# Performance work log

Hardware: AMD Instinct MI355X
Metric: run time of the kernel (lower is better)

Reference implementation:

```python
import jax, jax.numpy as jnp
import numpy as np

E, B, D, H, Z = 8, 16384, 512, 512, 64   # experts, batch, input_dim, hidden, latent
NHID = 2                                 # num_mlp_layers - 1 hidden-to-hidden layers


def setup_inputs() -> dict:
    key = jax.random.key(0)
    ks = jax.random.split(key, 12)

    def w(k, shape, fan_in):
        return (jax.random.normal(k, shape, jnp.float32) / np.sqrt(fan_in)).astype(jnp.float32)

    return {
        "x": jax.random.normal(ks[0], (B, D), jnp.float32),
        "eps": jax.random.normal(ks[1], (B, Z), jnp.float32),
        # stacked per-expert parameters (leading axis E)
        "enc_in_w": w(ks[2], (E, D, H), D), "enc_in_b": jnp.zeros((E, H), jnp.float32),
        "enc_hid_w": w(ks[3], (E, NHID, H, H), H), "enc_hid_b": jnp.zeros((E, NHID, H), jnp.float32),
        "mu_w": w(ks[4], (E, H, Z), H), "mu_b": jnp.zeros((E, Z), jnp.float32),
        "lv_w": w(ks[5], (E, H, Z), H), "lv_b": jnp.zeros((E, Z), jnp.float32),
        "dec_in_w": w(ks[6], (E, Z, H), Z), "dec_in_b": jnp.zeros((E, H), jnp.float32),
        "dec_hid_w": w(ks[7], (E, NHID, H, H), H), "dec_hid_b": jnp.zeros((E, NHID, H), jnp.float32),
        "dec_out_w": w(ks[8], (E, H, D), H), "dec_out_b": jnp.zeros((E, D), jnp.float32),
    }


def _moe_forward(x, eps, enc_in_w, enc_in_b, enc_hid_w, enc_hid_b,
                 mu_w, mu_b, lv_w, lv_b,
                 dec_in_w, dec_in_b, dec_hid_w, dec_hid_b, dec_out_w, dec_out_b):
    # ---- every expert tries the problem (dense, all experts over full batch) ----
    h = jax.nn.relu(jnp.einsum('bd,edh->ebh', x, enc_in_w) + enc_in_b[:, None, :])
    for i in range(NHID):
        h = jax.nn.relu(jnp.einsum('ebh,ehk->ebk', h, enc_hid_w[:, i]) + enc_hid_b[:, i, None, :])
    mu = jnp.einsum('ebh,ehz->ebz', h, mu_w) + mu_b[:, None, :]          # [E,B,Z]
    logvar = jnp.einsum('ebh,ehz->ebz', h, lv_w) + lv_b[:, None, :]       # [E,B,Z]
    z = mu + jnp.exp(0.5 * logvar) * eps[None, :, :]                      # reparameterize
    g = jax.nn.relu(jnp.einsum('ebz,ezh->ebh', z, dec_in_w) + dec_in_b[:, None, :])
    for i in range(NHID):
        g = jax.nn.relu(jnp.einsum('ebh,ehk->ebk', g, dec_hid_w[:, i]) + dec_hid_b[:, i, None, :])
    xhat = jnp.einsum('ebh,ehd->ebd', g, dec_out_w) + dec_out_b[:, None, :]  # [E,B,D]

    # ---- per-sample recon loss, pick best expert (torch.min over experts) ----
    recon = jnp.mean((xhat - x[None, :, :]) ** 2, axis=-1)                # [E,B]
    expert_idx = jnp.argmin(recon, axis=0)                                # [B]

    # ---- sparse_others: single fused gather instead of python loop ----
    bi = jnp.arange(x.shape[0])
    return mu[expert_idx, bi], logvar[expert_idx, bi], xhat[expert_idx, bi]


def reference(x, eps, enc_in_w, enc_in_b, enc_hid_w, enc_hid_b,
              mu_w, mu_b, lv_w, lv_b,
              dec_in_w, dec_in_b, dec_hid_w, dec_hid_b, dec_out_w, dec_out_b):
    return _moe_forward(x, eps, enc_in_w, enc_in_b, enc_hid_w, enc_hid_b,
                        mu_w, mu_b, lv_w, lv_b,
                        dec_in_w, dec_in_b, dec_hid_w, dec_hid_b, dec_out_w, dec_out_b)
```

## Files before the change

### kernel.cpp

```cpp
#include <hip/hip_runtime.h>
#include <cstdint>

#define Eexp 8
#define Bb   16384
#define Dd   512
#define Hh   512
#define Zz   64

typedef _Float16 f16x8 __attribute__((ext_vector_type(8)));
typedef float    f32x4 __attribute__((ext_vector_type(4)));

#define OFF_ENCIN  0
#define OFF_HID0   524288
#define OFF_HID1   1048576
#define OFF_HEADS  1572864
#define OFF_DECIN  1703936
#define OFF_DHID0  1769472
#define OFF_DHID1  2293760
#define OFF_DECOUT 2818048
#define PEREXP     3342336
#define WT_TOTAL   (8 * (size_t)PEREXP)

template<bool TR>
__global__ __launch_bounds__(256)
void fmsplit(const float* __restrict__ src, _Float16* __restrict__ dst,
             int KTOT, int inner, long sStride, long dStride)
{
    __shared__ float t[64][65];
    const int e  = blockIdx.z;
    const int o0 = blockIdx.x * 64;
    const int k0 = blockIdx.y * 64;
    const float* S = src + (size_t)e * sStride;
    _Float16*    D = dst + (size_t)e * dStride;
    const int tid = threadIdx.x;
    const int rr = tid >> 4, c4 = (tid & 15) * 4;
    #pragma unroll
    for (int p = 0; p < 4; ++p) {
        const int r = rr + p * 16;
        const float4 v = *reinterpret_cast<const float4*>(
            S + (size_t)(TR ? (k0 + r) : (o0 + r)) * inner + (TR ? o0 : k0) + c4);
        t[r][c4 + 0] = v.x; t[r][c4 + 1] = v.y;
        t[r][c4 + 2] = v.z; t[r][c4 + 3] = v.w;
    }
    __syncthreads();
    const int lane = tid & 63, wid = tid >> 6;
    #pragma unroll
    for (int p = 0; p < 2; ++p) {
        const int g  = wid * 2 + p;
        const int ot = g >> 1, kb = g & 1;
        const int ridx  = ot * 16 + (lane & 15);
        const int kbase = kb * 32 + (lane >> 4) * 8;
        f16x8 hv, lvv;
        #pragma unroll
        for (int j = 0; j < 8; ++j) {
            const float v = TR ? t[kbase + j][ridx] : t[ridx][kbase + j];
            const _Float16 h = (_Float16)v;
            hv[j]  = h;
            lvv[j] = (_Float16)(v - (float)h);
        }
        const size_t base =
            ((size_t)((o0 >> 4) + ot) * (KTOT >> 5) + (k0 >> 5) + kb) * 1024;
        *reinterpret_cast<f16x8*>(D + base + lane * 8)       = hv;
        *reinterpret_cast<f16x8*>(D + base + 512 + lane * 8) = lvv;
    }
}

__global__ __launch_bounds__(256)
void zfm_kernel(const float* __restrict__ mu, const float* __restrict__ lv,
                const float* __restrict__ eps, _Float16* __restrict__ zfm)
{
    __shared__ float t[64][65];
    const int r0 = blockIdx.x * 64;
    const int tid = threadIdx.x, rr = tid >> 4, c4 = (tid & 15) * 4;
    #pragma unroll
    for (int p = 0; p < 4; ++p) {
        const int r = rr + p * 16;
        const size_t o = (size_t)(r0 + r) * 64 + c4;
        const float4 m = *reinterpret_cast<const float4*>(mu + o);
        const float4 l = *reinterpret_cast<const float4*>(lv + o);
        const float4 e = *reinterpret_cast<const float4*>(eps + o);
        t[r][c4 + 0] = m.x + expf(0.5f * l.x) * e.x;
        t[r][c4 + 1] = m.y + expf(0.5f * l.y) * e.y;
        t[r][c4 + 2] = m.z + expf(0.5f * l.z) * e.z;
        t[r][c4 + 3] = m.w + expf(0.5f * l.w) * e.w;
    }
    __syncthreads();
    const int lane = tid & 63, wid = tid >> 6;
    #pragma unroll
    for (int p = 0; p < 2; ++p) {
        const int g  = wid * 2 + p;
        const int ot = g >> 1, kb = g & 1;
        const int ridx  = ot * 16 + (lane & 15);
        const int kbase = kb * 32 + (lane >> 4) * 8;
        f16x8 hv, lvv;
        #pragma unroll
        for (int j = 0; j < 8; ++j) {
            const float v = t[ridx][kbase + j];
            const _Float16 h = (_Float16)v;
            hv[j]  = h;
            lvv[j] = (_Float16)(v - (float)h);
        }
        const size_t base = ((size_t)((r0 >> 4) + ot) * 2 + kb) * 1024;
        *reinterpret_cast<f16x8*>(zfm + base + lane * 8)       = hv;
        *reinterpret_cast<f16x8*>(zfm + base + 512 + lane * 8) = lvv;
    }
}

template<int KA, int MODE>
__global__ __launch_bounds__(256, 3)
void gemm6(const _Float16* __restrict__ Afm, const _Float16* __restrict__ Wfm,
           const float* __restrict__ bias0, const float* __restrict__ bias1,
           float* __restrict__ Cf, float* __restrict__ Cf1,
           _Float16* __restrict__ Cfm,
           const float* __restrict__ Xin, float* __restrict__ rec8)
{
    constexpr int nY = (MODE == 2) ? 1 : 4;
    constexpr int KB = KA / 32;
    __shared__ uint32_t sb[(MODE == 0) ? 2 * 4096 : 64];

    int wg = blockIdx.x;
    wg = (wg & 7) * ((int)gridDim.x >> 3) + (wg >> 3);
    const int bx = wg / nY, by = wg % nY;

    const int lane = threadIdx.x & 63, wid = threadIdx.x >> 6;
    const int wr = wid >> 1, wc = wid & 1;
    const int row0 = bx * 128, col0 = by * 128;
    const int rt0 = (row0 >> 4) + wr * 4;
    const int ct0 = (col0 >> 4) + wc * 4;

    const _Float16* aBase = Afm + (size_t)rt0 * KB * 1024 + lane * 8;
    const _Float16* wBase = Wfm + (size_t)ct0 * KB * 1024 + lane * 8;

    f32x4 acc[4][4];
    #pragma unroll
    for (int i = 0; i < 4; ++i)
        #pragma unroll
        for (int j = 0; j < 4; ++j) acc[i][j] = {0.f, 0.f, 0.f, 0.f};

    for (int kb = 0; kb < KB; ++kb) {
        f16x8 ah[4], al[4], wh[4], wl[4];
        #pragma unroll
        for (int mf = 0; mf < 4; ++mf) {
            const _Float16* p = aBase + ((size_t)mf * KB + kb) * 1024;
            ah[mf] = *reinterpret_cast<const f16x8*>(p);
            al[mf] = *reinterpret_cast<const f16x8*>(p + 512);
        }
        #pragma unroll
        for (int nf = 0; nf < 4; ++nf) {
            const _Float16* p = wBase + ((size_t)nf * KB + kb) * 1024;
            wh[nf] = *reinterpret_cast<const f16x8*>(p);
            wl[nf] = *reinterpret_cast<const f16x8*>(p + 512);
        }
        #pragma unroll
        for (int mf = 0; mf < 4; ++mf)
            #pragma unroll
            for (int nf = 0; nf < 4; ++nf) {
                acc[mf][nf] = __builtin_amdgcn_mfma_f32_16x16x32_f16(
                    ah[mf], wh[nf], acc[mf][nf], 0, 0, 0);
                acc[mf][nf] = __builtin_amdgcn_mfma_f32_16x16x32_f16(
                    ah[mf], wl[nf], acc[mf][nf], 0, 0, 0);
                acc[mf][nf] = __builtin_amdgcn_mfma_f32_16x16x32_f16(
                    al[mf], wh[nf], acc[mf][nf], 0, 0, 0);
            }
    }

    if (MODE == 0) {
        #pragma unroll
        for (int p = 0; p < 2; ++p) {
            if (wc == p) {
                #pragma unroll
                for (int nf = 0; nf < 4; ++nf) {
                    const int col = nf * 16 + (lane & 15);
                    const float bv = bias0[col0 + wc * 64 + col];
                    #pragma unroll
                    for (int mf = 0; mf < 4; ++mf)
                        #pragma unroll
                        for (int j = 0; j < 4; ++j) {
                            const int lrow = mf * 16 + (lane >> 4) * 4 + j;
                            const float v = fmaxf(acc[mf][nf][j] + bv, 0.f);
                            const _Float16 h = (_Float16)v;
                            const _Float16 l = (_Float16)(v - (float)h);
                            const uint32_t pk =
                                (uint32_t)__builtin_bit_cast(uint16_t, h) |
                                ((uint32_t)__builtin_bit_cast(uint16_t, l) << 16);
                            const int chunk = (col >> 2) ^ (lrow & 15);
                            sb[wr * 4096 + lrow * 64 + chunk * 4 + (col & 3)] = pk;
                        }
                }
            }
            __syncthreads();
            if (wc == p) {
                #pragma unroll
                for (int t4 = 0; t4 < 4; ++t4)
                    #pragma unroll
                    for (int kb2 = 0; kb2 < 2; ++kb2) {
                        const int lrow = t4 * 16 + (lane & 15);
                        uint32_t u[8];
                        #pragma unroll
                        for (int jb = 0; jb < 2; ++jb) {
                            const int chunk =
                                (kb2 * 8 + (lane >> 4) * 2 + jb) ^ (lrow & 15);
                            const uint32_t* pp =
                                &sb[wr * 4096 + lrow * 64 + chunk * 4];
                            u[jb * 4 + 0] = pp[0]; u[jb * 4 + 1] = pp[1];
                            u[jb * 4 + 2] = pp[2]; u[jb * 4 + 3] = pp[3];
                        }
                        f16x8 hv, lvv;
                        #pragma unroll
                        for (int j = 0; j < 8; ++j) {
                            hv[j]  = __builtin_bit_cast(_Float16, (uint16_t)(u[j] & 0xffff));
                            lvv[j] = __builtin_bit_cast(_Float16, (uint16_t)(u[j] >> 16));
                        }
                        const int gtile = (row0 >> 4) + wr * 4 + t4;
                        const int gkb   = (col0 >> 5) + wc * 2 + kb2;
                        const size_t base = ((size_t)gtile * 16 + gkb) * 1024;
                        *reinterpret_cast<f16x8*>(Cfm + base + lane * 8)       = hv;
                        *reinterpret_cast<f16x8*>(Cfm + base + 512 + lane * 8) = lvv;
                    }
            }
            __syncthreads();
        }
    } else if (MODE == 1) {
        float rsum[4][4];
        #pragma unroll
        for (int mf = 0; mf < 4; ++mf)
            #pragma unroll
            for (int j = 0; j < 4; ++j) rsum[mf][j] = 0.f;
        #pragma unroll
        for (int nf = 0; nf < 4; ++nf) {
            const int col = col0 + wc * 64 + nf * 16 + (lane & 15);
            const float bv = bias0[col];
            #pragma unroll
            for (int mf = 0; mf < 4; ++mf)
                #pragma unroll
                for (int j = 0; j < 4; ++j) {
                    const int row = row0 + wr * 64 + mf * 16 + (lane >> 4) * 4 + j;
                    const float v = acc[mf][nf][j] + bv;
                    Cf[(size_t)row * 512 + col] = v;
                    const float d = v - Xin[(size_t)row * 512 + col];
                    rsum[mf][j] += d * d;
                }
        }
        #pragma unroll
        for (int mf = 0; mf < 4; ++mf)
            #pragma unroll
            for (int j = 0; j < 4; ++j) {
                float s = rsum[mf][j];
                s += __shfl_xor(s, 1); s += __shfl_xor(s, 2);
                s += __shfl_xor(s, 4); s += __shfl_xor(s, 8);
                if ((lane & 15) == 0) {
                    const int row = row0 + wr * 64 + mf * 16 + (lane >> 4) * 4 + j;
                    rec8[(size_t)(by * 2 + wc) * Bb + row] = s;
                }
            }
    } else {
        #pragma unroll
        for (int nf = 0; nf < 4; ++nf) {
            const int colq = wc * 64 + nf * 16 + (lane & 15);
            const float bv = (colq < 64) ? bias0[colq] : bias1[colq - 64];
            float* CP = (colq < 64) ? Cf : Cf1;
            const int c = colq & 63;
            #pragma unroll
            for (int mf = 0; mf < 4; ++mf)
                #pragma unroll
                for (int j = 0; j < 4; ++j) {
                    const int row = row0 + wr * 64 + mf * 16 + (lane >> 4) * 4 + j;
                    CP[(size_t)row * 64 + c] = acc[mf][nf][j] + bv;
                }
        }
    }
}

__global__ __launch_bounds__(256)
void select_kernel(const float* __restrict__ rec8, float* __restrict__ best,
                   const float* __restrict__ mu_e, const float* __restrict__ lv_e,
                   const float* __restrict__ xhat,
                   float* __restrict__ out_mu, float* __restrict__ out_lv,
                   float* __restrict__ out_xh, int isFirst)
{
    const int wave = threadIdx.x >> 6;
    const int lane = threadIdx.x & 63;
    const int row  = blockIdx.x * 4 + wave;
    float r = 0.f;
    #pragma unroll
    for (int p = 0; p < 8; ++p) r += rec8[(size_t)p * Bb + row];
    r *= (1.0f / 512.0f);
    const bool cond = isFirst || (r < best[row]);
    if (cond) {
        if (lane == 0) best[row] = r;
        out_mu[(size_t)row * Zz + lane] = mu_e[(size_t)row * Zz + lane];
        out_lv[(size_t)row * Zz + lane] = lv_e[(size_t)row * Zz + lane];
        const float4* src = reinterpret_cast<const float4*>(&xhat[(size_t)row * Dd]);
        float4*       dst = reinterpret_cast<float4*>(&out_xh[(size_t)row * Dd]);
        dst[lane]      = src[lane];
        dst[lane + 64] = src[lane + 64];
    }
}

extern "C" void kernel_launch(void* const* d_in, const int* in_sizes, int n_in,
                              void* d_out, int out_size, void* d_ws, size_t ws_size,
                              hipStream_t stream)
{
    const float* x         = (const float*)d_in[0];
    const float* eps       = (const float*)d_in[1];
    const float* enc_in_w  = (const float*)d_in[2];
    const float* enc_in_b  = (const float*)d_in[3];
    const float* enc_hid_w = (const float*)d_in[4];
    const float* enc_hid_b = (const float*)d_in[5];
    const float* mu_w      = (const float*)d_in[6];
    const float* mu_b      = (const float*)d_in[7];
    const float* lv_w      = (const float*)d_in[8];
    const float* lv_b      = (const float*)d_in[9];
    const float* dec_in_w  = (const float*)d_in[10];
    const float* dec_in_b  = (const float*)d_in[11];
    const float* dec_hid_w = (const float*)d_in[12];
    const float* dec_hid_b = (const float*)d_in[13];
    const float* dec_out_w = (const float*)d_in[14];
    const float* dec_out_b = (const float*)d_in[15];

    const size_t FM = (size_t)Bb * 512 * 2;
    const size_t BZ = (size_t)Bb * 64;

    _Float16* wt  = (_Float16*)d_ws;
    _Float16* xfm = wt + WT_TOTAL;
    _Float16* afm = xfm + FM;
    _Float16* bfm = afm + FM;
    _Float16* zfm = bfm + FM;
    float* fbase  = (float*)(zfm + (size_t)Bb * 64 * 2);
    float* xhat   = fbase;
    float* mu_e   = xhat + (size_t)Bb * 512;
    float* lv_e   = mu_e + BZ;
    float* rec8   = lv_e + BZ;
    float* best   = rec8 + (size_t)8 * Bb;

    float* out_mu = (float*)d_out;
    float* out_lv = out_mu + (size_t)Bb * Zz;
    float* out_xh = out_lv + (size_t)Bb * Zz;

    const dim3 blk(256);

    fmsplit<true ><<<dim3(8, 8, 8), blk, 0, stream>>>(enc_in_w,           wt + OFF_ENCIN,  512, 512, 262144, PEREXP);
    fmsplit<true ><<<dim3(8, 8, 8), blk, 0, stream>>>(enc_hid_w,          wt + OFF_HID0,   512, 512, 524288, PEREXP);
    fmsplit<true ><<<dim3(8, 8, 8), blk, 0, stream>>>(enc_hid_w + 262144, wt + OFF_HID1,   512, 512, 524288, PEREXP);
    fmsplit<true ><<<dim3(1, 8, 8), blk, 0, stream>>>(mu_w,               wt + OFF_HEADS,  512,  64,  32768, PEREXP);
    fmsplit<true ><<<dim3(1, 8, 8), blk, 0, stream>>>(lv_w,   wt + OFF_HEADS + 65536,      512,  64,  32768, PEREXP);
    fmsplit<true ><<<dim3(8, 1, 8), blk, 0, stream>>>(dec_in_w,           wt + OFF_DECIN,   64, 512,  32768, PEREXP);
    fmsplit<true ><<<dim3(8, 8, 8), blk, 0, stream>>>(dec_hid_w,          wt + OFF_DHID0,  512, 512, 524288, PEREXP);
    fmsplit<true ><<<dim3(8, 8, 8), blk, 0, stream>>>(dec_hid_w + 262144, wt + OFF_DHID1,  512, 512, 524288, PEREXP);
    fmsplit<true ><<<dim3(8, 8, 8), blk, 0, stream>>>(dec_out_w,          wt + OFF_DECOUT, 512, 512, 262144, PEREXP);
    fmsplit<false><<<dim3(256, 8, 1), blk, 0, stream>>>(x,                xfm,             512, 512, 0, 0);

    const dim3 gBig(512), gHead(128), gRow(Bb / 4), gZ(Bb / 64);

    for (int e = 0; e < Eexp; ++e) {
        const _Float16* we = wt + (size_t)e * PEREXP;
        gemm6<512, 0><<<gBig, blk, 0, stream>>>(
            xfm, we + OFF_ENCIN, enc_in_b + (size_t)e * Hh, nullptr,
            nullptr, nullptr, afm, nullptr, nullptr);
        gemm6<512, 0><<<gBig, blk, 0, stream>>>(
            afm, we + OFF_HID0, enc_hid_b + ((size_t)e * 2 + 0) * Hh, nullptr,
            nullptr, nullptr, bfm, nullptr, nullptr);
        gemm6<512, 0><<<gBig, blk, 0, stream>>>(
            bfm, we + OFF_HID1, enc_hid_b + ((size_t)e * 2 + 1) * Hh, nullptr,
            nullptr, nullptr, afm, nullptr, nullptr);
        gemm6<512, 2><<<gHead, blk, 0, stream>>>(
            afm, we + OFF_HEADS, mu_b + (size_t)e * Zz, lv_b + (size_t)e * Zz,
            mu_e, lv_e, nullptr, nullptr, nullptr);
        zfm_kernel<<<gZ, blk, 0, stream>>>(mu_e, lv_e, eps, zfm);
        gemm6< 64, 0><<<gBig, blk, 0, stream>>>(
            zfm, we + OFF_DECIN, dec_in_b + (size_t)e * Hh, nullptr,
            nullptr, nullptr, bfm, nullptr, nullptr);
        gemm6<512, 0><<<gBig, blk, 0, stream>>>(
            bfm, we + OFF_DHID0, dec_hid_b + ((size_t)e * 2 + 0) * Hh, nullptr,
            nullptr, nullptr, afm, nullptr, nullptr);
        gemm6<512, 0><<<gBig, blk, 0, stream>>>(
            afm, we + OFF_DHID1, dec_hid_b + ((size_t)e * 2 + 1) * Hh, nullptr,
            nullptr, nullptr, bfm, nullptr, nullptr);
        gemm6<512, 1><<<gBig, blk, 0, stream>>>(
            bfm, we + OFF_DECOUT, dec_out_b + (size_t)e * Dd, nullptr,
            xhat, nullptr, nullptr, x, rec8);
        select_kernel<<<gRow, blk, 0, stream>>>(
            rec8, best, mu_e, lv_e, xhat, out_mu, out_lv, out_xh, e == 0 ? 1 : 0);
    }
}
```

Before: 1.891 ms.

## Rewrite GEMM with 32x32 MFMA, LDS-staged weights and double-buffered pipeline

Replaces the 16x16x32 MFMA GEMM with one built on 32x32x16 MFMA, using 512-thread blocks and a fragment-major layout regrouped into 32-row, 16-k tiles. Weight tiles are staged into LDS through global_load_lds double buffering, and activation fragments are register double-buffered, with explicit waitcnt/barrier ordering and setprio around the MFMA bursts. The aim is to reuse weight tiles across waves and to overlap global loads with compute, so redundant per-wave global weight loads go away. In exchange the code carries tighter hand-written synchronisation, and the block-index swizzle for L2 locality is removed.

Result: slower. 2.057 ms (+8.8%).

```diff
diff --git a/kernel.cpp b/kernel.cpp
--- a/kernel.cpp
+++ b/kernel.cpp
@@ -7,8 +7,8 @@
 #define Hh   512
 #define Zz   64
 
-typedef _Float16 f16x8 __attribute__((ext_vector_type(8)));
-typedef float    f32x4 __attribute__((ext_vector_type(4)));
+typedef _Float16 f16x8  __attribute__((ext_vector_type(8)));
+typedef float    f32x16 __attribute__((ext_vector_type(16)));
 
 #define OFF_ENCIN  0
 #define OFF_HID0   524288
@@ -20,6 +20,10 @@
 #define OFF_DECOUT 2818048
 #define PEREXP     3342336
 #define WT_TOTAL   (8 * (size_t)PEREXP)
+
+#define GLL16(g, l) __builtin_amdgcn_global_load_lds( \
+    (const __attribute__((address_space(1))) void*)(g), \
+    (__attribute__((address_space(3))) void*)(l), 16, 0, 0)
 
 template<bool TR>
 __global__ __launch_bounds__(256)
@@ -44,24 +48,23 @@
     }
     __syncthreads();
     const int lane = tid & 63, wid = tid >> 6;
+    const int KB = KTOT >> 4;
     #pragma unroll
     for (int p = 0; p < 2; ++p) {
         const int g  = wid * 2 + p;
-        const int ot = g >> 1, kb = g & 1;
-        const int ridx  = ot * 16 + (lane & 15);
-        const int kbase = kb * 32 + (lane >> 4) * 8;
-        f16x8 hv, lvv;
+        const int ot = g >> 2, kk = g & 3;
+        const int rI = ot * 32 + (lane & 31);
+        const int kI = kk * 16 + (lane >> 5) * 8;
+        f16x8 hv, lv;
         #pragma unroll
         for (int j = 0; j < 8; ++j) {
-            const float v = TR ? t[kbase + j][ridx] : t[ridx][kbase + j];
+            const float v = TR ? t[kI + j][rI] : t[rI][kI + j];
             const _Float16 h = (_Float16)v;
-            hv[j]  = h;
-            lvv[j] = (_Float16)(v - (float)h);
+            hv[j] = h; lv[j] = (_Float16)(v - (float)h);
         }
-        const size_t base =
-            ((size_t)((o0 >> 4) + ot) * (KTOT >> 5) + (k0 >> 5) + kb) * 1024;
+        const size_t base = ((size_t)((o0 >> 5) + ot) * KB + (k0 >> 4) + kk) * 1024;
         *reinterpret_cast<f16x8*>(D + base + lane * 8)       = hv;
-        *reinterpret_cast<f16x8*>(D + base + 512 + lane * 8) = lvv;
+        *reinterpret_cast<f16x8*>(D + base + 512 + lane * 8) = lv;
     }
 }
 
@@ -89,121 +92,188 @@
     #pragma unroll
     for (int p = 0; p < 2; ++p) {
         const int g  = wid * 2 + p;
-        const int ot = g >> 1, kb = g & 1;
-        const int ridx  = ot * 16 + (lane & 15);
-        const int kbase = kb * 32 + (lane >> 4) * 8;
+        const int ot = g >> 2, kk = g & 3;
+        const int rI = ot * 32 + (lane & 31);
+        const int kI = kk * 16 + (lane >> 5) * 8;
         f16x8 hv, lvv;
         #pragma unroll
         for (int j = 0; j < 8; ++j) {
-            const float v = t[ridx][kbase + j];
+            const float v = t[rI][kI + j];
             const _Float16 h = (_Float16)v;
-            hv[j]  = h;
-            lvv[j] = (_Float16)(v - (float)h);
+            hv[j] = h; lvv[j] = (_Float16)(v - (float)h);
         }
-        const size_t base = ((size_t)((r0 >> 4) + ot) * 2 + kb) * 1024;
+        const size_t base = ((size_t)((r0 >> 5) + ot) * 4 + kk) * 1024;
         *reinterpret_cast<f16x8*>(zfm + base + lane * 8)       = hv;
         *reinterpret_cast<f16x8*>(zfm + base + 512 + lane * 8) = lvv;
     }
 }
 
 template<int KA, int MODE>
-__global__ __launch_bounds__(256, 3)
-void gemm6(const _Float16* __restrict__ Afm, const _Float16* __restrict__ Wfm,
+__global__ __launch_bounds__(512, 2)
+void gemm7(const _Float16* __restrict__ Afm, const _Float16* __restrict__ Wfm,
            const float* __restrict__ bias0, const float* __restrict__ bias1,
            float* __restrict__ Cf, float* __restrict__ Cf1,
            _Float16* __restrict__ Cfm,
            const float* __restrict__ Xin, float* __restrict__ rec8)
 {
-    constexpr int nY = (MODE == 2) ? 1 : 4;
-    constexpr int KB = KA / 32;
-    __shared__ uint32_t sb[(MODE == 0) ? 2 * 4096 : 64];
-
-    int wg = blockIdx.x;
-    wg = (wg & 7) * ((int)gridDim.x >> 3) + (wg >> 3);
+    constexpr int TM   = (MODE == 2) ? 1 : 2;
+    constexpr int TN   = (MODE == 2) ? 1 : 2;
+    constexpr int nY   = (MODE == 2) ? 2 : 4;
+    constexpr int BN32 = (MODE == 2) ? 2 : 4;
+    constexpr int KB   = KA / 16;
+    constexpr int NT   = KA / 32;
+    constexpr int CH   = BN32 * 4;
+    constexpr int CPW  = CH / 8;
+    constexpr int LDSB = (MODE == 0) ? 65536 : 2 * CH * 1024;
+    __shared__ __align__(16) uint8_t lds_raw[LDSB];
+    _Float16* sW = reinterpret_cast<_Float16*>(lds_raw);
+
+    const int wg = blockIdx.x;
     const int bx = wg / nY, by = wg % nY;
-
     const int lane = threadIdx.x & 63, wid = threadIdx.x >> 6;
     const int wr = wid >> 1, wc = wid & 1;
-    const int row0 = bx * 128, col0 = by * 128;
-    const int rt0 = (row0 >> 4) + wr * 4;
-    const int ct0 = (col0 >> 4) + wc * 4;
-
-    const _Float16* aBase = Afm + (size_t)rt0 * KB * 1024 + lane * 8;
-    const _Float16* wBase = Wfm + (size_t)ct0 * KB * 1024 + lane * 8;
-
-    f32x4 acc[4][4];
-    #pragma unroll
-    for (int i = 0; i < 4; ++i)
-        #pragma unroll
-        for (int j = 0; j < 4; ++j) acc[i][j] = {0.f, 0.f, 0.f, 0.f};
-
-    for (int kb = 0; kb < KB; ++kb) {
-        f16x8 ah[4], al[4], wh[4], wl[4];
-        #pragma unroll
-        for (int mf = 0; mf < 4; ++mf) {
-            const _Float16* p = aBase + ((size_t)mf * KB + kb) * 1024;
-            ah[mf] = *reinterpret_cast<const f16x8*>(p);
-            al[mf] = *reinterpret_cast<const f16x8*>(p + 512);
-        }
-        #pragma unroll
-        for (int nf = 0; nf < 4; ++nf) {
-            const _Float16* p = wBase + ((size_t)nf * KB + kb) * 1024;
-            wh[nf] = *reinterpret_cast<const f16x8*>(p);
-            wl[nf] = *reinterpret_cast<const f16x8*>(p + 512);
-        }
-        #pragma unroll
-        for (int mf = 0; mf < 4; ++mf)
+
+    const int rt0  = bx * (TM * 4) + wr * TM;
+    const int ct0  = by * BN32;
+    const int col0 = by * (BN32 * 32);
+
+    const _Float16* wSrc[CPW];
+    #pragma unroll
+    for (int p = 0; p < CPW; ++p) {
+        const int q  = wid * CPW + p;
+        const int wt = q >> 2, s = (q >> 1) & 1, pl = q & 1;
+        wSrc[p] = Wfm + ((size_t)(ct0 + wt) * KB + s) * 1024 + pl * 512 + lane * 8;
+    }
+    const _Float16* aSrc[TM];
+    #pragma unroll
+    for (int mf = 0; mf < TM; ++mf)
+        aSrc[mf] = Afm + (size_t)(rt0 + mf) * KB * 1024 + lane * 8;
+
+    f32x16 acc[TM][TN];
+    #pragma unroll
+    for (int i = 0; i < TM; ++i)
+        #pragma unroll
+        for (int j = 0; j < TN; ++j)
             #pragma unroll
-            for (int nf = 0; nf < 4; ++nf) {
-                acc[mf][nf] = __builtin_amdgcn_mfma_f32_16x16x32_f16(
-                    ah[mf], wh[nf], acc[mf][nf], 0, 0, 0);
-                acc[mf][nf] = __builtin_amdgcn_mfma_f32_16x16x32_f16(
-                    ah[mf], wl[nf], acc[mf][nf], 0, 0, 0);
-                acc[mf][nf] = __builtin_amdgcn_mfma_f32_16x16x32_f16(
-                    al[mf], wh[nf], acc[mf][nf], 0, 0, 0);
-            }
-    }
-
-    if (MODE == 0) {
-        #pragma unroll
-        for (int p = 0; p < 2; ++p) {
-            if (wc == p) {
+            for (int r = 0; r < 16; ++r) acc[i][j][r] = 0.f;
+
+    f16x8 aRegA[TM][2][2], aRegB[TM][2][2];
+
+#define STAGE_W(buf)                                                          \
+    { _Pragma("unroll")                                                       \
+      for (int p = 0; p < CPW; ++p) {                                         \
+          GLL16(wSrc[p], sW + (buf) * (CH * 512) + (wid * CPW + p) * 512);    \
+          wSrc[p] += 2048;                                                    \
+      } }
+
+#define LOAD_A(dst)                                                           \
+    { _Pragma("unroll")                                                       \
+      for (int mf = 0; mf < TM; ++mf) {                                       \
+          _Pragma("unroll")                                                   \
+          for (int s = 0; s < 2; ++s)                                         \
+              _Pragma("unroll")                                               \
+              for (int pl = 0; pl < 2; ++pl)                                  \
+                  dst[mf][s][pl] = *reinterpret_cast<const f16x8*>(           \
+                      aSrc[mf] + s * 1024 + pl * 512);                        \
+          aSrc[mf] += 2048;                                                   \
+      } }
+
+    STAGE_W(0)
+    LOAD_A(aRegA)
+    if (NT > 1) STAGE_W(1)
+
+#define ITER(t, buf, aCur, aNxt)                                              \
+    {                                                                         \
+        if ((t) + 1 < NT) {                                                   \
+            if constexpr (CPW == 2)                                           \
+                asm volatile("s_waitcnt vmcnt(2)" ::: "memory");              \
+            else                                                              \
+                asm volatile("s_waitcnt vmcnt(1)" ::: "memory");              \
+        } else {                                                              \
+            asm volatile("s_waitcnt vmcnt(0)" ::: "memory");                  \
+        }                                                                     \
+        __builtin_amdgcn_s_barrier();                                         \
+        asm volatile("" ::: "memory");                                        \
+        if ((t) + 1 < NT) LOAD_A(aNxt)                                        \
+        f16x8 wf[TN][2][2];                                                   \
+        _Pragma("unroll")                                                     \
+        for (int nf = 0; nf < TN; ++nf)                                       \
+            _Pragma("unroll")                                                 \
+            for (int s = 0; s < 2; ++s)                                       \
+                _Pragma("unroll")                                             \
+                for (int pl = 0; pl < 2; ++pl)                                \
+                    wf[nf][s][pl] = *reinterpret_cast<const f16x8*>(          \
+                        sW + (buf) * (CH * 512) +                             \
+                        (((wc * TN + nf) * 2 + s) * 2 + pl) * 512 + lane * 8);\
+        __builtin_amdgcn_s_setprio(1);                                        \
+        _Pragma("unroll")                                                     \
+        for (int s = 0; s < 2; ++s)                                           \
+            _Pragma("unroll")                                                 \
+            for (int mf = 0; mf < TM; ++mf)                                   \
+                _Pragma("unroll")                                             \
+                for (int nf = 0; nf < TN; ++nf) {                             \
+                    acc[mf][nf] = __builtin_amdgcn_mfma_f32_32x32x16_f16(     \
+                        aCur[mf][s][0], wf[nf][s][0], acc[mf][nf], 0, 0, 0);  \
+                    acc[mf][nf] = __builtin_amdgcn_mfma_f32_32x32x16_f16(     \
+                        aCur[mf][s][0], wf[nf][s][1], acc[mf][nf], 0, 0, 0);  \
+                    acc[mf][nf] = __builtin_amdgcn_mfma_f32_32x32x16_f16(     \
+                        aCur[mf][s][1], wf[nf][s][0], acc[mf][nf], 0, 0, 0);  \
+                }                                                             \
+        __builtin_amdgcn_s_setprio(0);                                        \
+        asm volatile("" ::: "memory");                                        \
+        __builtin_amdgcn_s_barrier();                                         \
+        asm volatile("" ::: "memory");                                        \
+        if ((t) + 2 < NT) STAGE_W(buf)                                        \
+    }
+
+    for (int t = 0; t < NT; t += 2) {
+        ITER(t,     0, aRegA, aRegB)
+        ITER(t + 1, 1, aRegB, aRegA)
+    }
+#undef ITER
+#undef LOAD_A
+#undef STAGE_W
+
+    if constexpr (MODE == 0) {
+        uint32_t* sb = reinterpret_cast<uint32_t*>(lds_raw);
+        #pragma unroll
+        for (int ph = 0; ph < 2; ++ph) {
+            if (wc == ph) {
                 #pragma unroll
-                for (int nf = 0; nf < 4; ++nf) {
-                    const int col = nf * 16 + (lane & 15);
-                    const float bv = bias0[col0 + wc * 64 + col];
+                for (int nf = 0; nf < 2; ++nf) {
+                    const float bv = bias0[col0 + wc * 64 + nf * 32 + (lane & 31)];
                     #pragma unroll
-                    for (int mf = 0; mf < 4; ++mf)
+                    for (int mf = 0; mf < 2; ++mf)
                         #pragma unroll
-                        for (int j = 0; j < 4; ++j) {
-                            const int lrow = mf * 16 + (lane >> 4) * 4 + j;
-                            const float v = fmaxf(acc[mf][nf][j] + bv, 0.f);
+                        for (int rg = 0; rg < 16; ++rg) {
+                            const int r_l = mf * 32 + (rg & 3) + 8 * (rg >> 2) + 4 * (lane >> 5);
+                            const int c_l = nf * 32 + (lane & 31);
+                            float v = fmaxf(acc[mf][nf][rg] + bv, 0.f);
                             const _Float16 h = (_Float16)v;
-                            const _Float16 l = (_Float16)(v - (float)h);
+                            const _Float16 lo = (_Float16)(v - (float)h);
                             const uint32_t pk =
                                 (uint32_t)__builtin_bit_cast(uint16_t, h) |
-                                ((uint32_t)__builtin_bit_cast(uint16_t, l) << 16);
-                            const int chunk = (col >> 2) ^ (lrow & 15);
-                            sb[wr * 4096 + lrow * 64 + chunk * 4 + (col & 3)] = pk;
+                                ((uint32_t)__builtin_bit_cast(uint16_t, lo) << 16);
+                            sb[wr * 4096 + r_l * 64 +
+                               ((((c_l >> 2) ^ (r_l & 15))) << 2) + (c_l & 3)] = pk;
                         }
                 }
             }
             __syncthreads();
-            if (wc == p) {
+            if (wc == ph) {
                 #pragma unroll
-                for (int t4 = 0; t4 < 4; ++t4)
+                for (int t32 = 0; t32 < 2; ++t32)
                     #pragma unroll
-                    for (int kb2 = 0; kb2 < 2; ++kb2) {
-                        const int lrow = t4 * 16 + (lane & 15);
+                    for (int kk = 0; kk < 4; ++kk) {
+                        const int r_l = t32 * 32 + (lane & 31);
+                        const int cb  = kk * 16 + (lane >> 5) * 8;
                         uint32_t u[8];
                         #pragma unroll
                         for (int jb = 0; jb < 2; ++jb) {
-                            const int chunk =
-                                (kb2 * 8 + (lane >> 4) * 2 + jb) ^ (lrow & 15);
-                            const uint32_t* pp =
-                                &sb[wr * 4096 + lrow * 64 + chunk * 4];
-                            u[jb * 4 + 0] = pp[0]; u[jb * 4 + 1] = pp[1];
-                            u[jb * 4 + 2] = pp[2]; u[jb * 4 + 3] = pp[3];
+                            const int chunk = ((cb >> 2) + jb) ^ (r_l & 15);
+                            const uint32_t* pp = &sb[wr * 4096 + r_l * 64 + chunk * 4];
+                            u[jb*4+0] = pp[0]; u[jb*4+1] = pp[1];
+                            u[jb*4+2] = pp[2]; u[jb*4+3] = pp[3];
                         }
                         f16x8 hv, lvv;
                         #pragma unroll
@@ -211,62 +281,58 @@
                             hv[j]  = __builtin_bit_cast(_Float16, (uint16_t)(u[j] & 0xffff));
                             lvv[j] = __builtin_bit_cast(_Float16, (uint16_t)(u[j] >> 16));
                         }
-                        const int gtile = (row0 >> 4) + wr * 4 + t4;
-                        const int gkb   = (col0 >> 5) + wc * 2 + kb2;
-                        const size_t base = ((size_t)gtile * 16 + gkb) * 1024;
-                        *reinterpret_cast<f16x8*>(Cfm + base + lane * 8)       = hv;
-                        *reinterpret_cast<f16x8*>(Cfm + base + 512 + lane * 8) = lvv;
+                        const int Tg = rt0 + t32;
+                        const int Sg = ((col0 + wc * 64) >> 4) + kk;
+                        _Float16* dst = Cfm + ((size_t)Tg * 32 + Sg) * 1024 + lane * 8;
+                        *reinterpret_cast<f16x8*>(dst)       = hv;
+                        *reinterpret_cast<f16x8*>(dst + 512) = lvv;
                     }
             }
             __syncthreads();
         }
-    } else if (MODE == 1) {
-        float rsum[4][4];
-        #pragma unroll
-        for (int mf = 0; mf < 4; ++mf)
+    } else if constexpr (MODE == 1) {
+        float rsum[2][16];
+        #pragma unroll
+        for (int mf = 0; mf < 2; ++mf)
             #pragma unroll
-            for (int j = 0; j < 4; ++j) rsum[mf][j] = 0.f;
-        #pragma unroll
-        for (int nf = 0; nf < 4; ++nf) {
-            const int col = col0 + wc * 64 + nf * 16 + (lane & 15);
+            for (int rg = 0; rg < 16; ++rg) rsum[mf][rg] = 0.f;
+        #pragma unroll
+        for (int nf = 0; nf < 2; ++nf) {
+            const int col = col0 + wc * 64 + nf * 32 + (lane & 31);
             const float bv = bias0[col];
             #pragma unroll
-            for (int mf = 0; mf < 4; ++mf)
+            for (int mf = 0; mf < 2; ++mf)
                 #pragma unroll
-                for (int j = 0; j < 4; ++j) {
-                    const int row = row0 + wr * 64 + mf * 16 + (lane >> 4) * 4 + j;
-                    const float v = acc[mf][nf][j] + bv;
+                for (int rg = 0; rg < 16; ++rg) {
+                    const int row = (rt0 + mf) * 32 + (rg & 3) + 8 * (rg >> 2) + 4 * (lane >> 5);
+                    const float v = acc[mf][nf][rg] + bv;
                     Cf[(size_t)row * 512 + col] = v;
                     const float d = v - Xin[(size_t)row * 512 + col];
-                    rsum[mf][j] += d * d;
+                    rsum[mf][rg] += d * d;
                 }
         }
         #pragma unroll
-        for (int mf = 0; mf < 4; ++mf)
+        for (int mf = 0; mf < 2; ++mf)
             #pragma unroll
-            for (int j = 0; j < 4; ++j) {
-                float s = rsum[mf][j];
-                s += __shfl_xor(s, 1); s += __shfl_xor(s, 2);
-                s += __shfl_xor(s, 4); s += __shfl_xor(s, 8);
-                if ((lane & 15) == 0) {
-                    const int row = row0 + wr * 64 + mf * 16 + (lane >> 4) * 4 + j;
+            for (int rg = 0; rg < 16; ++rg) {
+                float s = rsum[mf][rg];
+                s += __shfl_xor(s, 1);  s += __shfl_xor(s, 2);
+                s += __shfl_xor(s, 4);  s += __shfl_xor(s, 8);
+                s += __shfl_xor(s, 16);
+                if ((lane & 31) == 0) {
+                    const int row = (rt0 + mf) * 32 + (rg & 3) + 8 * (rg >> 2) + 4 * (lane >> 5);
                     rec8[(size_t)(by * 2 + wc) * Bb + row] = s;
                 }
             }
     } else {
-        #pragma unroll
-        for (int nf = 0; nf < 4; ++nf) {
-            const int colq = wc * 64 + nf * 16 + (lane & 15);
-            const float bv = (colq < 64) ? bias0[colq] : bias1[colq - 64];
-            float* CP = (colq < 64) ? Cf : Cf1;
-            const int c = colq & 63;
-            #pragma unroll
-            for (int mf = 0; mf < 4; ++mf)
-                #pragma unroll
-                for (int j = 0; j < 4; ++j) {
-                    const int row = row0 + wr * 64 + mf * 16 + (lane >> 4) * 4 + j;
-                    CP[(size_t)row * 64 + c] = acc[mf][nf][j] + bv;
-                }
+        const float* bP = (by == 0) ? bias0 : bias1;
+        float* CP = (by == 0) ? Cf : Cf1;
+        const int c = wc * 32 + (lane & 31);
+        const float bv = bP[c];
+        #pragma unroll
+        for (int rg = 0; rg < 16; ++rg) {
+            const int row = rt0 * 32 + (rg & 3) + 8 * (rg >> 2) + 4 * (lane >> 5);
+            CP[(size_t)row * 64 + c] = acc[0][0][rg] + bv;
         }
     }
 }
@@ -343,40 +409,40 @@
     fmsplit<true ><<<dim3(8, 8, 8), blk, 0, stream>>>(enc_hid_w,          wt + OFF_HID0,   512, 512, 524288, PEREXP);
     fmsplit<true ><<<dim3(8, 8, 8), blk, 0, stream>>>(enc_hid_w + 262144, wt + OFF_HID1,   512, 512, 524288, PEREXP);
     fmsplit<true ><<<dim3(1, 8, 8), blk, 0, stream>>>(mu_w,               wt + OFF_HEADS,  512,  64,  32768, PEREXP);
-    fmsplit<true ><<<dim3(1, 8, 8), blk, 0, stream>>>(lv_w,   wt + OFF_HEADS + 65536,      512,  64,  32768, PEREXP);
+    fmsplit<true ><<<dim3(1, 8, 8), blk, 0, stream>>>(lv_w,        wt + OFF_HEADS + 65536, 512,  64,  32768, PEREXP);
     fmsplit<true ><<<dim3(8, 1, 8), blk, 0, stream>>>(dec_in_w,           wt + OFF_DECIN,   64, 512,  32768, PEREXP);
     fmsplit<true ><<<dim3(8, 8, 8), blk, 0, stream>>>(dec_hid_w,          wt + OFF_DHID0,  512, 512, 524288, PEREXP);
     fmsplit<true ><<<dim3(8, 8, 8), blk, 0, stream>>>(dec_hid_w + 262144, wt + OFF_DHID1,  512, 512, 524288, PEREXP);
     fmsplit<true ><<<dim3(8, 8, 8), blk, 0, stream>>>(dec_out_w,          wt + OFF_DECOUT, 512, 512, 262144, PEREXP);
     fmsplit<false><<<dim3(256, 8, 1), blk, 0, stream>>>(x,                xfm,             512, 512, 0, 0);
 
-    const dim3 gBig(512), gHead(128), gRow(Bb / 4), gZ(Bb / 64);
+    const dim3 g256(256), gblk(512), gRow(Bb / 4), gZ(Bb / 64);
 
     for (int e = 0; e < Eexp; ++e) {
         const _Float16* we = wt + (size_t)e * PEREXP;
-        gemm6<512, 0><<<gBig, blk, 0, stream>>>(
+        gemm7<512, 0><<<g256, gblk, 0, stream>>>(
             xfm, we + OFF_ENCIN, enc_in_b + (size_t)e * Hh, nullptr,
             nullptr, nullptr, afm, nullptr, nullptr);
-        gemm6<512, 0><<<gBig, blk, 0, stream>>>(
+        gemm7<512, 0><<<g256, gblk, 0, stream>>>(
             afm, we + OFF_HID0, enc_hid_b + ((size_t)e * 2 + 0) * Hh, nullptr,
             nullptr, nullptr, bfm, nullptr, nullptr);
-        gemm6<512, 0><<<gBig, blk, 0, stream>>>(
+        gemm7<512, 0><<<g256, gblk, 0, stream>>>(
             bfm, we + OFF_HID1, enc_hid_b + ((size_t)e * 2 + 1) * Hh, nullptr,
             nullptr, nullptr, afm, nullptr, nullptr);
-        gemm6<512, 2><<<gHead, blk, 0, stream>>>(
+        gemm7<512, 2><<<g256, gblk, 0, stream>>>(
             afm, we + OFF_HEADS, mu_b + (size_t)e * Zz, lv_b + (size_t)e * Zz,
             mu_e, lv_e, nullptr, nullptr, nullptr);
         zfm_kernel<<<gZ, blk, 0, stream>>>(mu_e, lv_e, eps, zfm);
-        gemm6< 64, 0><<<gBig, blk, 0, stream>>>(
+        gemm7< 64, 0><<<g256, gblk, 0, stream>>>(
             zfm, we + OFF_DECIN, dec_in_b + (size_t)e * Hh, nullptr,
             nullptr, nullptr, bfm, nullptr, nullptr);
-        gemm6<512, 0><<<gBig, blk, 0, stream>>>(
+        gemm7<512, 0><<<g256, gblk, 0, stream>>>(
             bfm, we + OFF_DHID0, dec_hid_b + ((size_t)e * 2 + 0) * Hh, nullptr,
             nullptr, nullptr, afm, nullptr, nullptr);
-        gemm6<512, 0><<<gBig, blk, 0, stream>>>(
+        gemm7<512, 0><<<g256, gblk, 0, stream>>>(
             afm, we + OFF_DHID1, dec_hid_b + ((size_t)e * 2 + 1) * Hh, nullptr,
             nullptr, nullptr, bfm, nullptr, nullptr);
-        gemm6<512, 1><<<gBig, blk, 0, stream>>>(
+        gemm7<512, 1><<<g256, gblk, 0, stream>>>(
             bfm, we + OFF_DECOUT, dec_out_b + (size_t)e * Dd, nullptr,
             xhat, nullptr, nullptr, x, rec8);
         select_kernel<<<gRow, blk, 0, stream>>>(
```

## Stage GEMM tiles through LDS with async global-to-LDS double buffering

Applied to the files above, without the earlier changes.

Replaces the register-direct GEMM, in which each wave loaded its own fragments from global memory, with an 8-wave 256x128 block tile. The A and W fragments are staged into LDS through global_load_lds with double buffering, so they are shared across waves and the next K-slice load overlaps the MFMA work. It also adds s_setprio around the MFMA bursts and splits each K step into two phases to interleave loading and compute. The cost is more barriers per K step, a larger LDS footprint, and lower occupancy (2 blocks of 512 threads).

After: 2.000 ms. 1.06x slower.

```diff
diff --git a/kernel.cpp b/kernel.cpp
--- a/kernel.cpp
+++ b/kernel.cpp
@@ -8,6 +8,7 @@
 #define Zz   64
 
 typedef _Float16 f16x8 __attribute__((ext_vector_type(8)));
+typedef _Float16 f16x4 __attribute__((ext_vector_type(4)));
 typedef float    f32x4 __attribute__((ext_vector_type(4)));
 
 #define OFF_ENCIN  0
@@ -20,6 +21,10 @@
 #define OFF_DECOUT 2818048
 #define PEREXP     3342336
 #define WT_TOTAL   (8 * (size_t)PEREXP)
+
+#define GLL16(g, l) __builtin_amdgcn_global_load_lds( \
+    (const __attribute__((address_space(1))) void*)(g), \
+    (__attribute__((address_space(3))) void*)(l), 16, 0, 0)
 
 template<bool TR>
 __global__ __launch_bounds__(256)
@@ -44,24 +49,23 @@
     }
     __syncthreads();
     const int lane = tid & 63, wid = tid >> 6;
+    const int KB = KTOT >> 5;
     #pragma unroll
     for (int p = 0; p < 2; ++p) {
         const int g  = wid * 2 + p;
         const int ot = g >> 1, kb = g & 1;
-        const int ridx  = ot * 16 + (lane & 15);
-        const int kbase = kb * 32 + (lane >> 4) * 8;
-        f16x8 hv, lvv;
+        const int rI = ot * 16 + (lane & 15);
+        const int kI = kb * 32 + (lane >> 4) * 8;
+        f16x8 hv, lv;
         #pragma unroll
         for (int j = 0; j < 8; ++j) {
-            const float v = TR ? t[kbase + j][ridx] : t[ridx][kbase + j];
+            const float v = TR ? t[kI + j][rI] : t[rI][kI + j];
             const _Float16 h = (_Float16)v;
-            hv[j]  = h;
-            lvv[j] = (_Float16)(v - (float)h);
-        }
-        const size_t base =
-            ((size_t)((o0 >> 4) + ot) * (KTOT >> 5) + (k0 >> 5) + kb) * 1024;
+            hv[j] = h; lv[j] = (_Float16)(v - (float)h);
+        }
+        const size_t base = ((size_t)((o0 >> 4) + ot) * KB + (k0 >> 5) + kb) * 1024;
         *reinterpret_cast<f16x8*>(D + base + lane * 8)       = hv;
-        *reinterpret_cast<f16x8*>(D + base + 512 + lane * 8) = lvv;
+        *reinterpret_cast<f16x8*>(D + base + 512 + lane * 8) = lv;
     }
 }
 
@@ -90,15 +94,14 @@
     for (int p = 0; p < 2; ++p) {
         const int g  = wid * 2 + p;
         const int ot = g >> 1, kb = g & 1;
-        const int ridx  = ot * 16 + (lane & 15);
-        const int kbase = kb * 32 + (lane >> 4) * 8;
+        const int rI = ot * 16 + (lane & 15);
+        const int kI = kb * 32 + (lane >> 4) * 8;
         f16x8 hv, lvv;
         #pragma unroll
         for (int j = 0; j < 8; ++j) {
-            const float v = t[ridx][kbase + j];
+            const float v = t[rI][kI + j];
             const _Float16 h = (_Float16)v;
-            hv[j]  = h;
-            lvv[j] = (_Float16)(v - (float)h);
+            hv[j] = h; lvv[j] = (_Float16)(v - (float)h);
         }
         const size_t base = ((size_t)((r0 >> 4) + ot) * 2 + kb) * 1024;
         *reinterpret_cast<f16x8*>(zfm + base + lane * 8)       = hv;
@@ -107,54 +110,91 @@
 }
 
 template<int KA, int MODE>
-__global__ __launch_bounds__(256, 3)
-void gemm6(const _Float16* __restrict__ Afm, const _Float16* __restrict__ Wfm,
+__global__ __launch_bounds__(512, 2)
+void gemm8(const _Float16* __restrict__ Afm, const _Float16* __restrict__ Wfm,
            const float* __restrict__ bias0, const float* __restrict__ bias1,
            float* __restrict__ Cf, float* __restrict__ Cf1,
-           _Float16* __restrict__ Cfm,
-           const float* __restrict__ Xin, float* __restrict__ rec8)
+           _Float16* __restrict__ Cfm, const float* __restrict__ Xin,
+           float* __restrict__ rec8)
 {
-    constexpr int nY = (MODE == 2) ? 1 : 4;
-    constexpr int KB = KA / 32;
-    __shared__ uint32_t sb[(MODE == 0) ? 2 * 4096 : 64];
-
-    int wg = blockIdx.x;
-    wg = (wg & 7) * ((int)gridDim.x >> 3) + (wg >> 3);
-    const int bx = wg / nY, by = wg % nY;
+    constexpr bool BIG = (MODE != 2);
+    constexpr int BM  = BIG ? 256 : 64;
+    constexpr int KB  = KA / 32;
+    constexpr int NT  = KB;
+    constexpr int ACH = BIG ? 32 : 8;
+    constexpr int NCH = BIG ? 48 : 24;
+    constexpr int CPW = NCH / 8;
+    constexpr int NF  = BIG ? 4 : 1;
+    __shared__ __align__(16) _Float16 lds[2 * NCH * 512];
+
+    const int bid = blockIdx.x;
+    const int logical = (bid & 7) * 32 + (bid >> 3);
+    const int bx = BIG ? (logical & 63) : logical;
+    const int by = BIG ? (logical >> 6) : 0;
 
     const int lane = threadIdx.x & 63, wid = threadIdx.x >> 6;
-    const int wr = wid >> 1, wc = wid & 1;
-    const int row0 = bx * 128, col0 = by * 128;
-    const int rt0 = (row0 >> 4) + wr * 4;
-    const int ct0 = (col0 >> 4) + wc * 4;
-
-    const _Float16* aBase = Afm + (size_t)rt0 * KB * 1024 + lane * 8;
-    const _Float16* wBase = Wfm + (size_t)ct0 * KB * 1024 + lane * 8;
-
-    f32x4 acc[4][4];
+    const int wr = BIG ? (wid >> 1) : 0;
+    const int wc = BIG ? (wid & 1) : wid;
+    const int row0 = bx * BM;
+    const int col0 = by * 128;
+
+    const _Float16* src[CPW];
+    #pragma unroll
+    for (int p = 0; p < CPW; ++p) {
+        const int q = wid * CPW + p;
+        if (q < ACH) {
+            const int T = q >> 1, pl = q & 1;
+            src[p] = Afm + (size_t)((row0 >> 4) + T) * KB * 1024 + pl * 512 + lane * 8;
+        } else {
+            const int T = (q - ACH) >> 1, pl = q & 1;
+            src[p] = Wfm + (size_t)((col0 >> 4) + T) * KB * 1024 + pl * 512 + lane * 8;
+        }
+    }
+
+    f32x4 acc[4][NF];
     #pragma unroll
     for (int i = 0; i < 4; ++i)
         #pragma unroll
-        for (int j = 0; j < 4; ++j) acc[i][j] = {0.f, 0.f, 0.f, 0.f};
-
-    for (int kb = 0; kb < KB; ++kb) {
-        f16x8 ah[4], al[4], wh[4], wl[4];
+        for (int j = 0; j < NF; ++j) acc[i][j] = {0.f, 0.f, 0.f, 0.f};
+
+#define STAGE_H(buf, h)                                                      \
+    { _Pragma("unroll")                                                      \
+      for (int p = (h) * 3; p < ((h) ? CPW : 3); ++p) {                      \
+          GLL16(src[p], lds + (buf) * (NCH * 512) + (wid * CPW + p) * 512);  \
+          src[p] += 1024;                                                    \
+      } }
+
+    STAGE_H(0, 0) STAGE_H(0, 1)
+
+    for (int t = 0; t < NT; ++t) {
+        const int b = t & 1;
+        const _Float16* B0 = lds + b * (NCH * 512);
+
+        if (t + 1 < NT) STAGE_H(b ^ 1, 0)
+        if (t + 1 < NT) { asm volatile("s_waitcnt vmcnt(3)" ::: "memory"); }
+        else            { asm volatile("s_waitcnt vmcnt(0)" ::: "memory"); }
+        __builtin_amdgcn_s_barrier();
+        asm volatile("" ::: "memory");
+
+        f16x8 ah[4], al[4], wh[NF], wl[NF];
         #pragma unroll
         for (int mf = 0; mf < 4; ++mf) {
-            const _Float16* p = aBase + ((size_t)mf * KB + kb) * 1024;
-            ah[mf] = *reinterpret_cast<const f16x8*>(p);
-            al[mf] = *reinterpret_cast<const f16x8*>(p + 512);
-        }
-        #pragma unroll
-        for (int nf = 0; nf < 4; ++nf) {
-            const _Float16* p = wBase + ((size_t)nf * KB + kb) * 1024;
-            wh[nf] = *reinterpret_cast<const f16x8*>(p);
-            wl[nf] = *reinterpret_cast<const f16x8*>(p + 512);
-        }
+            const int q = (wr * 4 + mf) << 1;
+            ah[mf] = *reinterpret_cast<const f16x8*>(B0 + q * 512 + lane * 8);
+            al[mf] = *reinterpret_cast<const f16x8*>(B0 + q * 512 + 512 + lane * 8);
+        }
+        constexpr int NF0 = BIG ? 2 : 1;
+        #pragma unroll
+        for (int nf = 0; nf < NF0; ++nf) {
+            const int q = ACH + ((wc * NF + nf) << 1);
+            wh[nf] = *reinterpret_cast<const f16x8*>(B0 + q * 512 + lane * 8);
+            wl[nf] = *reinterpret_cast<const f16x8*>(B0 + q * 512 + 512 + lane * 8);
+        }
+        __builtin_amdgcn_s_setprio(1);
         #pragma unroll
         for (int mf = 0; mf < 4; ++mf)
             #pragma unroll
-            for (int nf = 0; nf < 4; ++nf) {
+            for (int nf = 0; nf < NF0; ++nf) {
                 acc[mf][nf] = __builtin_amdgcn_mfma_f32_16x16x32_f16(
                     ah[mf], wh[nf], acc[mf][nf], 0, 0, 0);
                 acc[mf][nf] = __builtin_amdgcn_mfma_f32_16x16x32_f16(
@@ -162,48 +202,78 @@
                 acc[mf][nf] = __builtin_amdgcn_mfma_f32_16x16x32_f16(
                     al[mf], wh[nf], acc[mf][nf], 0, 0, 0);
             }
-    }
-
-    if (MODE == 0) {
-        #pragma unroll
-        for (int p = 0; p < 2; ++p) {
-            if (wc == p) {
+        __builtin_amdgcn_s_setprio(0);
+        asm volatile("" ::: "memory");
+        __builtin_amdgcn_s_barrier();
+        asm volatile("" ::: "memory");
+
+        if constexpr (BIG) {
+            if (t + 1 < NT) STAGE_H(b ^ 1, 1)
+            #pragma unroll
+            for (int nf = 2; nf < 4; ++nf) {
+                const int q = ACH + ((wc * NF + nf) << 1);
+                wh[nf] = *reinterpret_cast<const f16x8*>(B0 + q * 512 + lane * 8);
+                wl[nf] = *reinterpret_cast<const f16x8*>(B0 + q * 512 + 512 + lane * 8);
+            }
+            __builtin_amdgcn_s_setprio(1);
+            #pragma unroll
+            for (int mf = 0; mf < 4; ++mf)
                 #pragma unroll
-                for (int nf = 0; nf < 4; ++nf) {
-                    const int col = nf * 16 + (lane & 15);
-                    const float bv = bias0[col0 + wc * 64 + col];
+                for (int nf = 2; nf < 4; ++nf) {
+                    acc[mf][nf] = __builtin_amdgcn_mfma_f32_16x16x32_f16(
+                        ah[mf], wh[nf], acc[mf][nf], 0, 0, 0);
+                    acc[mf][nf] = __builtin_amdgcn_mfma_f32_16x16x32_f16(
+                        ah[mf], wl[nf], acc[mf][nf], 0, 0, 0);
+                    acc[mf][nf] = __builtin_amdgcn_mfma_f32_16x16x32_f16(
+                        al[mf], wh[nf], acc[mf][nf], 0, 0, 0);
+                }
+            __builtin_amdgcn_s_setprio(0);
+            asm volatile("" ::: "memory");
+            __builtin_amdgcn_s_barrier();
+            asm volatile("" ::: "memory");
+        }
+    }
+#undef STAGE_H
+
+    if constexpr (MODE == 0) {
+        uint32_t* sb = reinterpret_cast<uint32_t*>(&lds[0]);
+        #pragma unroll
+        for (int ph = 0; ph < 2; ++ph) {
+            if (wc == ph) {
+                #pragma unroll
+                for (int nf = 0; nf < NF; ++nf) {
+                    const int c_l = nf * 16 + (lane & 15);
+                    const float bv = bias0[col0 + wc * 64 + c_l];
                     #pragma unroll
                     for (int mf = 0; mf < 4; ++mf)
                         #pragma unroll
                         for (int j = 0; j < 4; ++j) {
-                            const int lrow = mf * 16 + (lane >> 4) * 4 + j;
+                            const int r_l = wr * 64 + mf * 16 + (lane >> 4) * 4 + j;
                             const float v = fmaxf(acc[mf][nf][j] + bv, 0.f);
                             const _Float16 h = (_Float16)v;
-                            const _Float16 l = (_Float16)(v - (float)h);
+                            const _Float16 lo = (_Float16)(v - (float)h);
                             const uint32_t pk =
                                 (uint32_t)__builtin_bit_cast(uint16_t, h) |
-                                ((uint32_t)__builtin_bit_cast(uint16_t, l) << 16);
-                            const int chunk = (col >> 2) ^ (lrow & 15);
-                            sb[wr * 4096 + lrow * 64 + chunk * 4 + (col & 3)] = pk;
+                                ((uint32_t)__builtin_bit_cast(uint16_t, lo) << 16);
+                            sb[r_l * 64 + (((c_l >> 2) ^ (r_l & 15)) << 2) + (c_l & 3)] = pk;
                         }
                 }
             }
             __syncthreads();
-            if (wc == p) {
+            if (wc == ph) {
                 #pragma unroll
-                for (int t4 = 0; t4 < 4; ++t4)
+                for (int T_l = 0; T_l < 4; ++T_l)
                     #pragma unroll
-                    for (int kb2 = 0; kb2 < 2; ++kb2) {
-                        const int lrow = t4 * 16 + (lane & 15);
+                    for (int kb_l = 0; kb_l < 2; ++kb_l) {
+                        const int r_l = wr * 64 + T_l * 16 + (lane & 15);
+                        const int cb  = kb_l * 32 + (lane >> 4) * 8;
                         uint32_t u[8];
                         #pragma unroll
                         for (int jb = 0; jb < 2; ++jb) {
-                            const int chunk =
-                                (kb2 * 8 + (lane >> 4) * 2 + jb) ^ (lrow & 15);
-                            const uint32_t* pp =
-                                &sb[wr * 4096 + lrow * 64 + chunk * 4];
-                            u[jb * 4 + 0] = pp[0]; u[jb * 4 + 1] = pp[1];
-                            u[jb * 4 + 2] = pp[2]; u[jb * 4 + 3] = pp[3];
+                            const int chunk = ((cb >> 2) + jb) ^ (r_l & 15);
+                            const uint32_t* pp = &sb[r_l * 64 + chunk * 4];
+                            u[jb*4+0] = pp[0]; u[jb*4+1] = pp[1];
+                            u[jb*4+2] = pp[2]; u[jb*4+3] = pp[3];
                         }
                         f16x8 hv, lvv;
                         #pragma unroll
@@ -211,23 +281,23 @@
                             hv[j]  = __builtin_bit_cast(_Float16, (uint16_t)(u[j] & 0xffff));
                             lvv[j] = __builtin_bit_cast(_Float16, (uint16_t)(u[j] >> 16));
                         }
-                        const int gtile = (row0 >> 4) + wr * 4 + t4;
-                        const int gkb   = (col0 >> 5) + wc * 2 + kb2;
-                        const size_t base = ((size_t)gtile * 16 + gkb) * 1024;
+                        const size_t base =
+                            ((size_t)((row0 >> 4) + wr * 4 + T_l) * 16 +
+                             (col0 >> 5) + wc * 2 + kb_l) * 1024;
                         *reinterpret_cast<f16x8*>(Cfm + base + lane * 8)       = hv;
                         *reinterpret_cast<f16x8*>(Cfm + base + 512 + lane * 8) = lvv;
                     }
             }
             __syncthreads();
         }
-    } else if (MODE == 1) {
+    } else if constexpr (MODE == 1) {
         float rsum[4][4];
         #pragma unroll
         for (int mf = 0; mf < 4; ++mf)
             #pragma unroll
             for (int j = 0; j < 4; ++j) rsum[mf][j] = 0.f;
         #pragma unroll
-        for (int nf = 0; nf < 4; ++nf) {
+        for (int nf = 0; nf < NF; ++nf) {
             const int col = col0 + wc * 64 + nf * 16 + (lane & 15);
             const float bv = bias0[col];
             #pragma unroll
@@ -254,20 +324,17 @@
                 }
             }
     } else {
-        #pragma unroll
-        for (int nf = 0; nf < 4; ++nf) {
-            const int colq = wc * 64 + nf * 16 + (lane & 15);
-            const float bv = (colq < 64) ? bias0[colq] : bias1[colq - 64];
-            float* CP = (colq < 64) ? Cf : Cf1;
-            const int c = colq & 63;
-            #pragma unroll
-            for (int mf = 0; mf < 4; ++mf)
-                #pragma unroll
-                for (int j = 0; j < 4; ++j) {
-                    const int row = row0 + wr * 64 + mf * 16 + (lane >> 4) * 4 + j;
-                    CP[(size_t)row * 64 + c] = acc[mf][nf][j] + bv;
-                }
-        }
+        const int c_h = wc * 16 + (lane & 15);
+        const float bv = (c_h < 64) ? bias0[c_h] : bias1[c_h - 64];
+        float* CP = (c_h < 64) ? Cf : Cf1;
+        const int c = c_h & 63;
+        #pragma unroll
+        for (int mf = 0; mf < 4; ++mf)
+            #pragma unroll
+            for (int j = 0; j < 4; ++j) {
+                const int row = row0 + mf * 16 + (lane >> 4) * 4 + j;
+                CP[(size_t)row * 64 + c] = acc[mf][0][j] + bv;
+            }
     }
 }
 
@@ -343,40 +410,40 @@
     fmsplit<true ><<<dim3(8, 8, 8), blk, 0, stream>>>(enc_hid_w,          wt + OFF_HID0,   512, 512, 524288, PEREXP);
     fmsplit<true ><<<dim3(8, 8, 8), blk, 0, stream>>>(enc_hid_w + 262144, wt + OFF_HID1,   512, 512, 524288, PEREXP);
     fmsplit<true ><<<dim3(1, 8, 8), blk, 0, stream>>>(mu_w,               wt + OFF_HEADS,  512,  64,  32768, PEREXP);
-    fmsplit<true ><<<dim3(1, 8, 8), blk, 0, stream>>>(lv_w,   wt + OFF_HEADS + 65536,      512,  64,  32768, PEREXP);
+    fmsplit<true ><<<dim3(1, 8, 8), blk, 0, stream>>>(lv_w,        wt + OFF_HEADS + 65536, 512,  64,  32768, PEREXP);
     fmsplit<true ><<<dim3(8, 1, 8), blk, 0, stream>>>(dec_in_w,           wt + OFF_DECIN,   64, 512,  32768, PEREXP);
     fmsplit<true ><<<dim3(8, 8, 8), blk, 0, stream>>>(dec_hid_w,          wt + OFF_DHID0,  512, 512, 524288, PEREXP);
     fmsplit<true ><<<dim3(8, 8, 8), blk, 0, stream>>>(dec_hid_w + 262144, wt + OFF_DHID1,  512, 512, 524288, PEREXP);
     fmsplit<true ><<<dim3(8, 8, 8), blk, 0, stream>>>(dec_out_w,          wt + OFF_DECOUT, 512, 512, 262144, PEREXP);
     fmsplit<false><<<dim3(256, 8, 1), blk, 0, stream>>>(x,                xfm,             512, 512, 0, 0);
 
-    const dim3 gBig(512), gHead(128), gRow(Bb / 4), gZ(Bb / 64);
+    const dim3 g256(256), gblk(512), gRow(Bb / 4), gZ(Bb / 64);
 
     for (int e = 0; e < Eexp; ++e) {
         const _Float16* we = wt + (size_t)e * PEREXP;
-        gemm6<512, 0><<<gBig, blk, 0, stream>>>(
+        gemm8<512, 0><<<g256, gblk, 0, stream>>>(
             xfm, we + OFF_ENCIN, enc_in_b + (size_t)e * Hh, nullptr,
             nullptr, nullptr, afm, nullptr, nullptr);
-        gemm6<512, 0><<<gBig, blk, 0, stream>>>(
+        gemm8<512, 0><<<g256, gblk, 0, stream>>>(
             afm, we + OFF_HID0, enc_hid_b + ((size_t)e * 2 + 0) * Hh, nullptr,
             nullptr, nullptr, bfm, nullptr, nullptr);
-        gemm6<512, 0><<<gBig, blk, 0, stream>>>(
+        gemm8<512, 0><<<g256, gblk, 0, stream>>>(
             bfm, we + OFF_HID1, enc_hid_b + ((size_t)e * 2 + 1) * Hh, nullptr,
             nullptr, nullptr, afm, nullptr, nullptr);
-        gemm6<512, 2><<<gHead, blk, 0, stream>>>(
+        gemm8<512, 2><<<g256, gblk, 0, stream>>>(
             afm, we + OFF_HEADS, mu_b + (size_t)e * Zz, lv_b + (size_t)e * Zz,
             mu_e, lv_e, nullptr, nullptr, nullptr);
         zfm_kernel<<<gZ, blk, 0, stream>>>(mu_e, lv_e, eps, zfm);
-        gemm6< 64, 0><<<gBig, blk, 0, stream>>>(
+        gemm8< 64, 0><<<g256, gblk, 0, stream>>>(
             zfm, we + OFF_DECIN, dec_in_b + (size_t)e * Hh, nullptr,
             nullptr, nullptr, bfm, nullptr, nullptr);
-        gemm6<512, 0><<<gBig, blk, 0, stream>>>(
+        gemm8<512, 0><<<g256, gblk, 0, stream>>>(
             bfm, we + OFF_DHID0, dec_hid_b + ((size_t)e * 2 + 0) * Hh, nullptr,
             nullptr, nullptr, afm, nullptr, nullptr);
-        gemm6<512, 0><<<gBig, blk, 0, stream>>>(
+        gemm8<512, 0><<<g256, gblk, 0, stream>>>(
             afm, we + OFF_DHID1, dec_hid_b + ((size_t)e * 2 + 1) * Hh, nullptr,
             nullptr, nullptr, bfm, nullptr, nullptr);
-        gemm6<512, 1><<<gBig, blk, 0, stream>>>(
+        gemm8<512, 1><<<g256, gblk, 0, stream>>>(
             bfm, we + OFF_DECOUT, dec_out_b + (size_t)e * Dd, nullptr,
             xhat, nullptr, nullptr, x, rec8);
         select_kernel<<<gRow, blk, 0, stream>>>(
```
